# Kernel optimization log

Measured on AMD Instinct MI355X. Metric: run time of the kernel, lower is better.

The kernel has to match this reference:

```python
import jax, jax.numpy as jnp
import numpy as np

NF = 16            # num_frequencies
S = 2              # scale_factor
MAX_STD = 0.5
POS_LIMIT = 1.0


def setup_inputs() -> dict:
    key = jax.random.key(0)
    ks = jax.random.split(key, 8)
    B, G, H, W = 16, 256, 128, 128
    hidden, base = 1024, 256
    in_dim = (G + 2 * NF + 1) * S * S  # 4624
    # xavier-uniform-like scales
    lim1 = float(np.sqrt(6.0 / (hidden + in_dim)))
    lim2 = float(np.sqrt(6.0 / (base + hidden)))
    return {
        "position": jax.random.uniform(ks[0], (B, 4), dtype=jnp.float32),
        "gestalt": jax.random.normal(ks[1], (B, G), dtype=jnp.float32),
        "mask": jax.random.uniform(ks[2], (B, 1, H, W), dtype=jnp.float32),
        "depth": jax.random.normal(ks[3], (B, 1, H, W), dtype=jnp.float32),
        "weight1": jax.random.uniform(ks[4], (hidden, in_dim), minval=-lim1, maxval=lim1, dtype=jnp.float32),
        "bias1": jnp.zeros((hidden,), dtype=jnp.float32),
        "weight2": jax.random.uniform(ks[5], (base, hidden), minval=-lim2, maxval=lim2, dtype=jnp.float32),
        "bias2": jnp.zeros((base,), dtype=jnp.float32),
    }


def reference(position, gestalt, mask, depth, weight1, bias1, weight2, bias2):
    B, _, H, W = mask.shape
    # positional grids in [-1, 1], shapes (1,1,H,W)
    gx = (jnp.arange(W, dtype=jnp.float32) / (W - 1)) * 2 - 1
    gy = (jnp.arange(H, dtype=jnp.float32) / (H - 1)) * 2 - 1
    grid_y, grid_x = jnp.meshgrid(gy, gx, indexing="ij")
    grid_x = grid_x[None, None]
    grid_y = grid_y[None, None]

    x = jnp.clip(position[:, 0], -POS_LIMIT, POS_LIMIT)[:, None, None, None]
    y = jnp.clip(position[:, 1], -POS_LIMIT, POS_LIMIT)[:, None, None, None]
    min_std = 1.0 / min(H, W)
    std = 0.1 / jnp.clip(position[:, 3], min_std, MAX_STD)[:, None, None, None]
    std_y = std
    std_x = std * (W / H)

    half_pi = jnp.float32(np.pi / 2)
    ngx = (grid_x - x) * std_x * half_pi  # (B,1,H,W)
    ngy = (grid_y - y) * std_y * half_pi
    freqs = (2.0 ** jnp.arange(NF, dtype=jnp.float32))[None, :, None, None]
    cos_x = jnp.cos(ngx * freqs)  # (B,NF,H,W)
    cos_y = jnp.cos(ngy * freqs)
    # interleave: [cx0, cy0, cx1, cy1, ...]
    embedding = jnp.stack([cos_x, cos_y], axis=2).reshape(B, 2 * NF, H, W)

    inp = jnp.concatenate(
        [gestalt[:, :, None, None] * mask, embedding * mask, depth * mask], axis=1
    )  # (B,C,H,W)
    C = inp.shape[1]
    # space-to-depth patchify
    p = inp.reshape(B, C, H // S, S, W // S, S)
    p = p.transpose(0, 2, 4, 1, 3, 5).reshape(B * (H // S) * (W // S), C * S * S)

    h = p @ weight1.T + bias1
    h = h * jax.nn.sigmoid(h)  # SiLU
    o = h @ weight2.T + bias2
    return o.reshape(B, H // S, W // S, -1).transpose(0, 3, 1, 2)
```

## Files before the change

kernel.cpp:

```cpp
#include <hip/hip_runtime.h>
#include <cstdio>


#define NFREQ 16
#define BB 16
#define G 256
#define KIN 1156
#define K1 144
#define STAGE_U16 12800
#define NSTAGE 3

typedef unsigned short u16;
using bf16x8 = __bf16 __attribute__((ext_vector_type(8)));
using f32x16 = float __attribute__((ext_vector_type(16)));
using f32x4  = float __attribute__((ext_vector_type(4)));

__device__ __forceinline__ u16 f2bf(float f) {
  unsigned u = __float_as_uint(f);
  u += 0x7fffu + ((u >> 16) & 1u);
  return (u16)(u >> 16);
}
__device__ __forceinline__ unsigned pk2(float a, float b) {
  return (unsigned)f2bf(a) | ((unsigned)f2bf(b) << 16);
}
__device__ __forceinline__ unsigned pk2f(float a, float b) {
  unsigned ua = __float_as_uint(a) + 0x8000u;
  unsigned ub = __float_as_uint(b) + 0x8000u;
  return __builtin_amdgcn_perm(ub, ua, 0x07060302u);
}
__device__ __forceinline__ float silu(float h) {
  float e = __builtin_amdgcn_exp2f(h * -1.44269504088896f);
  return h * __builtin_amdgcn_rcpf(1.f + e);
}
__device__ __forceinline__ void gl_lds16(const u16* g, u16* l) {
  __builtin_amdgcn_global_load_lds(
      (const __attribute__((address_space(1))) void*)g,
      (__attribute__((address_space(3))) void*)l, 16, 0, 0);
}

__global__ void k_pre(const float* __restrict__ pos,
                      const float* __restrict__ gestalt,
                      const float* __restrict__ w1,
                      const float* __restrict__ w2,
                      const float* __restrict__ bias1,
                      float* __restrict__ cosx, float* __restrict__ cosy,
                      u16* __restrict__ B1F, u16* __restrict__ W2F) {
  const int bid = blockIdx.x;
  const int t = threadIdx.x;

  if (bid < 1024) {
    __shared__ float w1row[KIN];
    __shared__ float gestT[G * 17];
    __shared__ float psum[256];
    __shared__ float wg[64];
    const int n = bid;
    const float b1v = bias1[n];
#pragma unroll
    for (int i = t; i < KIN; i += 256) w1row[i] = w1[(size_t)n * KIN + i];
#pragma unroll
    for (int i = t; i < BB * G; i += 256) {
      int bb = i >> 8, c = i & 255;
      gestT[c * 17 + bb] = gestalt[i];
    }
    __syncthreads();
    {
      int bb = t & 15, j = (t >> 4) & 3, q = t >> 6;
      float acc = 0.f;
#pragma unroll 8
      for (int c = q * 64; c < q * 64 + 64; ++c)
        acc += gestT[c * 17 + bb] * w1row[4 * c + j];
      psum[t] = acc;
    }
    __syncthreads();
    if (t < 64) {
      int bb = t >> 2, j = t & 3;
      wg[t] = psum[j * 16 + bb] + psum[64 + j * 16 + bb] +
              psum[128 + j * 16 + bb] + psum[192 + j * 16 + bb];
    }
    __syncthreads();
    const int ch = n >> 5, l31n = n & 31;
    for (int c = t; c < BB * (K1 / 8); c += 256) {
      int bb = c / 18, kc = c - bb * 18;
      int k0 = kc * 8;
      float v[8];
#pragma unroll
      for (int i = 0; i < 8; ++i) {
        int k = k0 + i;
        float vv;
        if (k < 64)       vv = w1row[1024 + 8 * (k >> 2) + (k & 3)];
        else if (k < 128) { int kk = k - 64; vv = w1row[1024 + 8 * (kk >> 2) + 4 + (kk & 3)]; }
        else if (k < 132) vv = wg[bb * 4 + (k - 128)];
        else if (k < 136) vv = w1row[1152 + (k - 132)];
        else if (k == 136) vv = b1v;
        else              vv = 0.f;
        v[i] = vv;
      }
      uint4 u;
      u.x = pk2(v[0], v[1]); u.y = pk2(v[2], v[3]);
      u.z = pk2(v[4], v[5]); u.w = pk2(v[6], v[7]);
      size_t idx0 = ((((size_t)bb * 32 + ch) * 9 + (kc >> 1)) * 64 +
                     (kc & 1) * 32 + l31n) * 8;
      *(uint4*)(B1F + idx0) = u;
    }
  } else if (bid < 1152) {
    int e8 = (bid - 1024) * 256 + t;
    int lane = e8 & 63;
    int ct   = (e8 >> 6) & 7;
    int kc   = e8 >> 9;
    int n2 = ct * 32 + (lane & 31);
    int k2 = kc * 16 + (lane >> 5) * 8;
    const float* src = w2 + (size_t)n2 * 1024 + k2;
    uint4 u;
    u.x = pk2(src[0], src[1]); u.y = pk2(src[2], src[3]);
    u.z = pk2(src[4], src[5]); u.w = pk2(src[6], src[7]);
    *(uint4*)(W2F + (size_t)e8 * 8) = u;
  } else {
    int idx = (bid - 1152) * 256 + t;
    int table = idx >> 15;
    int rem = idx & 32767;
    int b = rem >> 11;
    int f = (rem >> 7) & 15;
    int c = rem & 127;
    float p0 = pos[b * 4 + 0];
    float p1 = pos[b * 4 + 1];
    float p3 = pos[b * 4 + 3];
    float x = fminf(fmaxf(p0, -1.f), 1.f);
    float y = fminf(fmaxf(p1, -1.f), 1.f);
    float stdv = 0.1f / fminf(fmaxf(p3, 0.0078125f), 0.5f);
    const float half_pi = 1.57079632679489661923f;
    float g = ((float)c / 127.0f) * 2.0f - 1.0f;
    float ng = (table == 0) ? ((g - x) * stdv) * half_pi
                            : ((g - y) * stdv) * half_pi;
    float freq = (float)(1 << f);
    float val = cosf(ng * freq);
    if (table == 0) cosx[(b * NFREQ + f) * 128 + c] = val;
    else            cosy[(b * NFREQ + f) * 128 + c] = val;
  }
}


__device__ __forceinline__ f32x16 mfma_bf16(bf16x8 a, bf16x8 b, f32x16 c) {
  return __builtin_amdgcn_mfma_f32_32x32x16_bf16(a, b, c, 0, 0, 0);
}

__device__ __forceinline__ void gemm1(const u16* afb, const bf16x8* bfr, int lane8,
                                      const f32x16& ZERO, f32x16& a1a, f32x16& a1b) {
  bf16x8 af0 = *(const bf16x8*)(afb + 0 * 512 + lane8);
  bf16x8 af1 = *(const bf16x8*)(afb + 1 * 512 + lane8);
  a1a = mfma_bf16(af0, bfr[0], ZERO);
  a1b = mfma_bf16(af1, bfr[1], ZERO);
#pragma unroll
  for (int ks = 1; ks < 4; ++ks) {
    bf16x8 afa = *(const bf16x8*)(afb + (2 * ks) * 512 + lane8);
    bf16x8 afc = *(const bf16x8*)(afb + (2 * ks + 1) * 512 + lane8);
    a1a = mfma_bf16(afa, bfr[2 * ks], a1a);
    a1b = mfma_bf16(afc, bfr[2 * ks + 1], a1b);
  }
  bf16x8 af8 = *(const bf16x8*)(afb + 8 * 512 + lane8);
  a1a = mfma_bf16(af8, bfr[8], a1a);
}

__device__ __forceinline__ void gemm2(const u16* wfb, int lane8,
                                      bf16x8 fA, bf16x8 fB, f32x16* acc2) {
#pragma unroll
  for (int ct = 0; ct < 8; ++ct) {
    bf16x8 wf = *(const bf16x8*)(wfb + ct * 512 + lane8);
    acc2[ct] = mfma_bf16(fA, wf, acc2[ct]);
  }
#pragma unroll
  for (int ct = 0; ct < 8; ++ct) {
    bf16x8 wf = *(const bf16x8*)(wfb + 4096 + ct * 512 + lane8);
    acc2[ct] = mfma_bf16(fB, wf, acc2[ct]);
  }
}

__device__ __forceinline__ void silupack(const f32x16& a1a, const f32x16& a1b,
                                         bf16x8& fragA, bf16x8& fragB) {
  unsigned d[8];
#pragma unroll
  for (int q = 0; q < 4; ++q) {
    float s0 = silu(a1a[4 * q + 0] + a1b[4 * q + 0]);
    float s1 = silu(a1a[4 * q + 1] + a1b[4 * q + 1]);
    float s2 = silu(a1a[4 * q + 2] + a1b[4 * q + 2]);
    float s3 = silu(a1a[4 * q + 3] + a1b[4 * q + 3]);
    d[2 * q]     = pk2f(s0, s1);
    d[2 * q + 1] = pk2f(s2, s3);
  }
  unsigned e0 = d[0], e1 = d[2];
  unsigned e2 = d[1], e3 = d[3];
  unsigned e4 = d[4], e5 = d[6];
  unsigned e6 = d[5], e7 = d[7];
  asm("v_permlane32_swap_b32 %0, %1" : "+v"(e0), "+v"(e1));
  asm("v_permlane32_swap_b32 %0, %1" : "+v"(e2), "+v"(e3));
  asm("v_permlane32_swap_b32 %0, %1" : "+v"(e4), "+v"(e5));
  asm("v_permlane32_swap_b32 %0, %1" : "+v"(e6), "+v"(e7));
  uint4 fav, fbv;
  fav.x = e0; fav.y = e2; fav.z = e1; fav.w = e3;
  fbv.x = e4; fbv.y = e6; fbv.z = e5; fbv.w = e7;
  fragA = __builtin_bit_cast(bf16x8, fav);
  fragB = __builtin_bit_cast(bf16x8, fbv);
}

__global__ __launch_bounds__(256, 2) void k_main(
    const u16* __restrict__ B1F, const u16* __restrict__ W2F,
    const float* __restrict__ mask, const float* __restrict__ depth,
    const float* __restrict__ cosx, const float* __restrict__ cosy,
    const float* __restrict__ bias2, float* __restrict__ out)
{
  __shared__ __align__(16) u16 sbuf[NSTAGE * STAGE_U16];
  float* stg = (float*)sbuf;

  const int tid = threadIdx.x;
  const int w = tid >> 6;
  const int lane = tid & 63;
  const int lane8 = lane * 8;
  const int l31 = lane & 31;
  const int lhi = lane >> 5;
  const int bswz = (blockIdx.x & 7) * 64 + (blockIdx.x >> 3);
  const int r0 = bswz * 128;
  const int b = r0 >> 12;
  const int oy0 = (r0 >> 6) & 63;

  {
    const float4* cx4 = (const float4*)(cosx + (size_t)b * 2048);
    ((float4*)stg)[tid]       = cx4[tid];
    ((float4*)stg)[tid + 256] = cx4[tid + 256];
    if (tid < 64)
      stg[2048 + tid] = cosy[((size_t)b * 16 + (tid >> 2)) * 128 + 2 * oy0 + (tid & 3)];
    if (tid < 128) {
      ((float4*)(stg + 2112))[tid] = ((const float4*)(mask  + ((size_t)b * 128 + 2 * oy0) * 128))[tid];
      ((float4*)(stg + 2624))[tid] = ((const float4*)(depth + ((size_t)b * 128 + 2 * oy0) * 128))[tid];
    }
  }
  __syncthreads();

  bf16x8 bfr[9];
  {
    const int r = w * 32 + l31;
    const int oyl = r >> 6, ox = r & 63;
    float m[4], dd[4];
#pragma unroll
    for (int j = 0; j < 4; ++j) {
      int sy = j >> 1, sx = j & 1;
      float mv = stg[2112 + (2 * oyl + sy) * 128 + 2 * ox + sx];
      m[j] = mv;
      dd[j] = stg[2624 + (2 * oyl + sy) * 128 + 2 * ox + sx] * mv;
    }
#pragma unroll
    for (int ks = 0; ks < 9; ++ks) {
      const int k0 = ks * 16 + lhi * 8;
      unsigned dwords[4];
#pragma unroll
      for (int h = 0; h < 4; ++h) {
        float v[2];
#pragma unroll
        for (int p = 0; p < 2; ++p) {
          const int k = k0 + 2 * h + p;
          float vv;
          if (k < 64) {
            const int f = k >> 2, j = k & 3;
            vv = m[j] * stg[f * 128 + 2 * ox + (j & 1)];
          } else if (k < 128) {
            const int kk = k - 64, f = kk >> 2, j = kk & 3;
            vv = m[j] * stg[2048 + f * 4 + 2 * oyl + (j >> 1)];
          } else if (k < 132) {
            vv = m[k - 128];
          } else if (k < 136) {
            vv = dd[k - 132];
          } else if (k == 136) {
            vv = 1.0f;
          } else {
            vv = 0.f;
          }
          v[p] = vv;
        }
        dwords[h] = pk2(v[0], v[1]);
      }
      uint4 u; u.x = dwords[0]; u.y = dwords[1]; u.z = dwords[2]; u.w = dwords[3];
      bfr[ks] = __builtin_bit_cast(bf16x8, u);
    }
  }
  __syncthreads();

  f32x16 acc2[8];
#pragma unroll
  for (int c = 0; c < 8; ++c)
#pragma unroll
    for (int i = 0; i < 16; ++i) acc2[c][i] = 0.f;

  f32x16 ZERO;
#pragma unroll
  for (int i = 0; i < 16; ++i) ZERO[i] = 0.f;

  const int naf = (w == 0) ? 3 : 2;
  const int wf0 = 9 + ((w + 3) & 3);
  const u16* apre = B1F + (size_t)b * 32 * 4608 + lane8;
  const u16* wpre = W2F + lane8;

  auto prefetchP = [&](u16* dst) {
#pragma unroll
    for (int j = 0; j < 3; ++j)
      if (j < naf) gl_lds16(apre + (w + 4 * j) * 512, dst + (w + 4 * j) * 512);
#pragma unroll
    for (int j = 0; j < 4; ++j) {
      const int c = wf0 + 4 * j;
      gl_lds16(wpre + (c - 9) * 512, dst + c * 512);
    }
    apre += 4608; wpre += 8192;
  };

  prefetchP(sbuf);
  prefetchP(sbuf + STAGE_U16);
  asm volatile("s_waitcnt vmcnt(6)" ::: "memory");
  __builtin_amdgcn_s_barrier();
  asm volatile("" ::: "memory");
  __builtin_amdgcn_sched_barrier(0);

  bf16x8 fragA, fragB;

  {
    f32x16 a1a, a1b;
    __builtin_amdgcn_s_setprio(1);
    gemm1(sbuf, bfr, lane8, ZERO, a1a, a1b);
    __builtin_amdgcn_s_setprio(0);
    asm volatile("s_waitcnt vmcnt(0)" ::: "memory");
    __builtin_amdgcn_s_barrier();
    asm volatile("" ::: "memory");
    __builtin_amdgcn_sched_barrier(0);
    prefetchP(sbuf + 2 * STAGE_U16);
    silupack(a1a, a1b, fragA, fragB);
  }

  int st = 1;
  for (int ch = 1; ch < 32; ++ch) {
    const u16* afb  = sbuf + st * STAGE_U16;
    const int  stp  = (st == 0) ? 2 : st - 1;
    const u16* wfbp = sbuf + stp * STAGE_U16 + 4608;

    f32x16 a1a, a1b;
    __builtin_amdgcn_s_setprio(1);
    gemm1(afb, bfr, lane8, ZERO, a1a, a1b);
    gemm2(wfbp, lane8, fragA, fragB, acc2);
    __builtin_amdgcn_s_setprio(0);

    asm volatile("s_waitcnt vmcnt(0)" ::: "memory");
    __builtin_amdgcn_s_barrier();
    asm volatile("" ::: "memory");
    __builtin_amdgcn_sched_barrier(0);

    if (ch + 2 < 32) {
      int s2 = st + 2; if (s2 >= NSTAGE) s2 -= NSTAGE;
      prefetchP(sbuf + s2 * STAGE_U16);
    }

    silupack(a1a, a1b, fragA, fragB);
    if (++st == NSTAGE) st = 0;
  }

  gemm2(sbuf + 1 * STAGE_U16 + 4608, lane8, fragA, fragB, acc2);

#pragma unroll
  for (int ct = 0; ct < 8; ++ct) {
    const int n2 = ct * 32 + l31;
    const float b2 = bias2[n2];
    float* ob = out + ((size_t)b * 256 + n2) * 4096;
#pragma unroll
    for (int q = 0; q < 4; ++q) {
      const int rl = w * 32 + 8 * q + 4 * lhi;
      const int oy = oy0 + (rl >> 6);
      const int ox = rl & 63;
      f32x4 v;
      v[0] = acc2[ct][4 * q + 0] + b2;
      v[1] = acc2[ct][4 * q + 1] + b2;
      v[2] = acc2[ct][4 * q + 2] + b2;
      v[3] = acc2[ct][4 * q + 3] + b2;
      *(f32x4*)(ob + oy * 64 + ox) = v;
    }
  }
}


extern "C" void kernel_launch(void* const* d_in, const int* in_sizes, int n_in,
                              void* d_out, int out_size, void* d_ws, size_t ws_size,
                              hipStream_t stream) {
  const float* pos     = (const float*)d_in[0];
  const float* gestalt = (const float*)d_in[1];
  const float* mask    = (const float*)d_in[2];
  const float* depth   = (const float*)d_in[3];
  const float* w1      = (const float*)d_in[4];
  const float* bias1   = (const float*)d_in[5];
  const float* w2      = (const float*)d_in[6];
  const float* bias2   = (const float*)d_in[7];
  float* out = (float*)d_out;

  const size_t NEED = 131072u + 131072u + 4718592u + 524288u;
  if (ws_size < NEED) {
    fprintf(stderr, "[kernel] ws_size=%zu < needed %zu — skipping launches\n",
            ws_size, NEED);
    return;
  }
  char* ws = (char*)d_ws;
  float* cosx = (float*)(ws);
  float* cosy = (float*)(ws + 131072);
  u16*   B1F  = (u16*)(ws + 262144);
  u16*   W2F  = (u16*)(ws + 262144 + 4718592);

  k_pre<<<1408, 256, 0, stream>>>(pos, gestalt, w1, w2, bias1, cosx, cosy, B1F, W2F);
  k_main<<<512, 256, 0, stream>>>(B1F, W2F, mask, depth, cosx, cosy, bias2, out);
}
```

Measured before the change: 158.4 us.

## Use 512-thread blocks with a six-stage pipeline and barriers every two chunks

Doubles the work per block from 128 to 256 output rows using eight waves, halving the grid to 256 blocks. This halves how often each W1/W2 weight chunk is reloaded across blocks. The LDS ring grows from three to six stages so prefetch runs three chunks ahead, and the full vmcnt(0)+barrier per chunk becomes a partial wait with a barrier every other chunk. The roughly 150 KB of LDS limits each CU to one block, so latency hiding relies on the deeper prefetch and the eight waves within one block rather than on a second co-resident block.

```diff
diff --git a/kernel.cpp b/kernel.cpp
--- a/kernel.cpp
+++ b/kernel.cpp
@@ -8,7 +8,7 @@
 #define KIN 1156
 #define K1 144
 #define STAGE_U16 12800
-#define NSTAGE 3
+#define NSTAGE 6
 
 typedef unsigned short u16;
 using bf16x8 = __bf16 __attribute__((ext_vector_type(8)));
@@ -201,7 +201,7 @@
   fragB = __builtin_bit_cast(bf16x8, fbv);
 }
 
-__global__ __launch_bounds__(256, 2) void k_main(
+__global__ __launch_bounds__(512, 2) void k_main(
     const u16* __restrict__ B1F, const u16* __restrict__ W2F,
     const float* __restrict__ mask, const float* __restrict__ depth,
     const float* __restrict__ cosx, const float* __restrict__ cosy,
@@ -216,20 +216,19 @@
   const int lane8 = lane * 8;
   const int l31 = lane & 31;
   const int lhi = lane >> 5;
-  const int bswz = (blockIdx.x & 7) * 64 + (blockIdx.x >> 3);
-  const int r0 = bswz * 128;
+  const int bswz = (blockIdx.x & 7) * 32 + (blockIdx.x >> 3);
+  const int r0 = bswz * 256;
   const int b = r0 >> 12;
   const int oy0 = (r0 >> 6) & 63;
 
   {
     const float4* cx4 = (const float4*)(cosx + (size_t)b * 2048);
-    ((float4*)stg)[tid]       = cx4[tid];
-    ((float4*)stg)[tid + 256] = cx4[tid + 256];
-    if (tid < 64)
-      stg[2048 + tid] = cosy[((size_t)b * 16 + (tid >> 2)) * 128 + 2 * oy0 + (tid & 3)];
-    if (tid < 128) {
-      ((float4*)(stg + 2112))[tid] = ((const float4*)(mask  + ((size_t)b * 128 + 2 * oy0) * 128))[tid];
-      ((float4*)(stg + 2624))[tid] = ((const float4*)(depth + ((size_t)b * 128 + 2 * oy0) * 128))[tid];
+    ((float4*)stg)[tid] = cx4[tid];
+    if (tid < 128)
+      stg[2048 + tid] = cosy[((size_t)b * 16 + (tid >> 3)) * 128 + 2 * oy0 + (tid & 7)];
+    if (tid < 256) {
+      ((float4*)(stg + 2176))[tid] = ((const float4*)(mask  + ((size_t)b * 128 + 2 * oy0) * 128))[tid];
+      ((float4*)(stg + 3200))[tid] = ((const float4*)(depth + ((size_t)b * 128 + 2 * oy0) * 128))[tid];
     }
   }
   __syncthreads();
@@ -242,9 +241,9 @@
 #pragma unroll
     for (int j = 0; j < 4; ++j) {
       int sy = j >> 1, sx = j & 1;
-      float mv = stg[2112 + (2 * oyl + sy) * 128 + 2 * ox + sx];
+      float mv = stg[2176 + (2 * oyl + sy) * 128 + 2 * ox + sx];
       m[j] = mv;
-      dd[j] = stg[2624 + (2 * oyl + sy) * 128 + 2 * ox + sx] * mv;
+      dd[j] = stg[3200 + (2 * oyl + sy) * 128 + 2 * ox + sx] * mv;
     }
 #pragma unroll
     for (int ks = 0; ks < 9; ++ks) {
@@ -262,7 +261,7 @@
             vv = m[j] * stg[f * 128 + 2 * ox + (j & 1)];
           } else if (k < 128) {
             const int kk = k - 64, f = kk >> 2, j = kk & 3;
-            vv = m[j] * stg[2048 + f * 4 + 2 * oyl + (j >> 1)];
+            vv = m[j] * stg[2048 + f * 8 + 2 * oyl + (j >> 1)];
           } else if (k < 132) {
             vv = m[k - 128];
           } else if (k < 136) {
@@ -292,49 +291,54 @@
 #pragma unroll
   for (int i = 0; i < 16; ++i) ZERO[i] = 0.f;
 
-  const int naf = (w == 0) ? 3 : 2;
-  const int wf0 = 9 + ((w + 3) & 3);
   const u16* apre = B1F + (size_t)b * 32 * 4608 + lane8;
   const u16* wpre = W2F + lane8;
 
   auto prefetchP = [&](u16* dst) {
-#pragma unroll
-    for (int j = 0; j < 3; ++j)
-      if (j < naf) gl_lds16(apre + (w + 4 * j) * 512, dst + (w + 4 * j) * 512);
-#pragma unroll
-    for (int j = 0; j < 4; ++j) {
-      const int c = wf0 + 4 * j;
-      gl_lds16(wpre + (c - 9) * 512, dst + c * 512);
-    }
+    gl_lds16(apre + w * 512, dst + w * 512);
+    if (w == 7) gl_lds16(apre + 8 * 512, dst + 8 * 512);
+    gl_lds16(wpre + w * 512, dst + (9 + w) * 512);
+    gl_lds16(wpre + (8 + w) * 512, dst + (17 + w) * 512);
     apre += 4608; wpre += 8192;
   };
 
   prefetchP(sbuf);
   prefetchP(sbuf + STAGE_U16);
-  asm volatile("s_waitcnt vmcnt(6)" ::: "memory");
-  __builtin_amdgcn_s_barrier();
-  asm volatile("" ::: "memory");
-  __builtin_amdgcn_sched_barrier(0);
+  prefetchP(sbuf + 2 * STAGE_U16);
 
   bf16x8 fragA, fragB;
 
   {
+    if (w == 7) asm volatile("s_waitcnt vmcnt(4)" ::: "memory");
+    else        asm volatile("s_waitcnt vmcnt(3)" ::: "memory");
+    __builtin_amdgcn_s_barrier();
+    asm volatile("" ::: "memory");
+    __builtin_amdgcn_sched_barrier(0);
+    prefetchP(sbuf + 3 * STAGE_U16);
+
     f32x16 a1a, a1b;
     __builtin_amdgcn_s_setprio(1);
     gemm1(sbuf, bfr, lane8, ZERO, a1a, a1b);
     __builtin_amdgcn_s_setprio(0);
-    asm volatile("s_waitcnt vmcnt(0)" ::: "memory");
-    __builtin_amdgcn_s_barrier();
-    asm volatile("" ::: "memory");
-    __builtin_amdgcn_sched_barrier(0);
-    prefetchP(sbuf + 2 * STAGE_U16);
     silupack(a1a, a1b, fragA, fragB);
   }
 
   int st = 1;
+  int stw = 4;
   for (int ch = 1; ch < 32; ++ch) {
+    if (!(ch & 1)) {
+      if (ch == 30) asm volatile("s_waitcnt vmcnt(0)" ::: "memory");
+      else if (w == 7) asm volatile("s_waitcnt vmcnt(4)" ::: "memory");
+      else             asm volatile("s_waitcnt vmcnt(3)" ::: "memory");
+      __builtin_amdgcn_s_barrier();
+      asm volatile("" ::: "memory");
+      __builtin_amdgcn_sched_barrier(0);
+    }
+    if (ch + 3 < 32) prefetchP(sbuf + stw * STAGE_U16);
+    stw = (stw + 1 == NSTAGE) ? 0 : stw + 1;
+
     const u16* afb  = sbuf + st * STAGE_U16;
-    const int  stp  = (st == 0) ? 2 : st - 1;
+    const int  stp  = (st == 0) ? NSTAGE - 1 : st - 1;
     const u16* wfbp = sbuf + stp * STAGE_U16 + 4608;
 
     f32x16 a1a, a1b;
@@ -343,18 +347,8 @@
     gemm2(wfbp, lane8, fragA, fragB, acc2);
     __builtin_amdgcn_s_setprio(0);
 
-    asm volatile("s_waitcnt vmcnt(0)" ::: "memory");
-    __builtin_amdgcn_s_barrier();
-    asm volatile("" ::: "memory");
-    __builtin_amdgcn_sched_barrier(0);
-
-    if (ch + 2 < 32) {
-      int s2 = st + 2; if (s2 >= NSTAGE) s2 -= NSTAGE;
-      prefetchP(sbuf + s2 * STAGE_U16);
-    }
-
     silupack(a1a, a1b, fragA, fragB);
-    if (++st == NSTAGE) st = 0;
+    st = (st + 1 == NSTAGE) ? 0 : st + 1;
   }
 
   gemm2(sbuf + 1 * STAGE_U16 + 4608, lane8, fragA, fragB, acc2);
@@ -406,5 +400,5 @@
   u16*   W2F  = (u16*)(ws + 262144 + 4718592);
 
   k_pre<<<1408, 256, 0, stream>>>(pos, gestalt, w1, w2, bias1, cosx, cosy, B1F, W2F);
-  k_main<<<512, 256, 0, stream>>>(B1F, W2F, mask, depth, cosx, cosy, bias2, out);
-}
+  k_main<<<256, 512, 0, stream>>>(B1F, W2F, mask, depth, cosx, cosy, bias2, out);
+}
```

Result: no change. 156.5 us (-1.2%).

## Warp-specialize k_main into GEMM1 producer and GEMM2 consumer wave groups

Applied to the files above, without the earlier changes.

The block grows from 4 to 12 waves. Four waves compute GEMM1 plus SiLU and hand packed bf16 fragments through a double-buffered LDS region. Eight waves consume them for GEMM2, each pair splitting the output columns in half. The LDS pipeline goes from 3 to 4 stages, and each group issues its own global-to-LDS loads. This is meant to overlap GEMM1 and GEMM2 across waves instead of serializing them in one wave, at the cost of extra LDS traffic for the fragments, more LDS per block, and fragile hand-counted vmcnt/barrier matching between the two groups.

```diff
diff --git a/kernel.cpp b/kernel.cpp
--- a/kernel.cpp
+++ b/kernel.cpp
@@ -8,7 +8,8 @@
 #define KIN 1156
 #define K1 144
 #define STAGE_U16 12800
-#define NSTAGE 3
+#define NSTAGE 4
+#define SB_U16 (NSTAGE * STAGE_U16)
 
 typedef unsigned short u16;
 using bf16x8 = __bf16 __attribute__((ext_vector_type(8)));
@@ -160,22 +161,8 @@
   a1a = mfma_bf16(af8, bfr[8], a1a);
 }
 
-__device__ __forceinline__ void gemm2(const u16* wfb, int lane8,
-                                      bf16x8 fA, bf16x8 fB, f32x16* acc2) {
-#pragma unroll
-  for (int ct = 0; ct < 8; ++ct) {
-    bf16x8 wf = *(const bf16x8*)(wfb + ct * 512 + lane8);
-    acc2[ct] = mfma_bf16(fA, wf, acc2[ct]);
-  }
-#pragma unroll
-  for (int ct = 0; ct < 8; ++ct) {
-    bf16x8 wf = *(const bf16x8*)(wfb + 4096 + ct * 512 + lane8);
-    acc2[ct] = mfma_bf16(fB, wf, acc2[ct]);
-  }
-}
-
 __device__ __forceinline__ void silupack(const f32x16& a1a, const f32x16& a1b,
-                                         bf16x8& fragA, bf16x8& fragB) {
+                                         uint4& fav, uint4& fbv) {
   unsigned d[8];
 #pragma unroll
   for (int q = 0; q < 4; ++q) {
@@ -194,37 +181,32 @@
   asm("v_permlane32_swap_b32 %0, %1" : "+v"(e2), "+v"(e3));
   asm("v_permlane32_swap_b32 %0, %1" : "+v"(e4), "+v"(e5));
   asm("v_permlane32_swap_b32 %0, %1" : "+v"(e6), "+v"(e7));
-  uint4 fav, fbv;
   fav.x = e0; fav.y = e2; fav.z = e1; fav.w = e3;
   fbv.x = e4; fbv.y = e6; fbv.z = e5; fbv.w = e7;
-  fragA = __builtin_bit_cast(bf16x8, fav);
-  fragB = __builtin_bit_cast(bf16x8, fbv);
-}
-
-__global__ __launch_bounds__(256, 2) void k_main(
+}
+
+__global__ __launch_bounds__(768, 3) void k_main(
     const u16* __restrict__ B1F, const u16* __restrict__ W2F,
     const float* __restrict__ mask, const float* __restrict__ depth,
     const float* __restrict__ cosx, const float* __restrict__ cosy,
     const float* __restrict__ bias2, float* __restrict__ out)
 {
-  __shared__ __align__(16) u16 sbuf[NSTAGE * STAGE_U16];
+  __shared__ __align__(16) u16 sbuf[NSTAGE * STAGE_U16 + 8192];
   float* stg = (float*)sbuf;
 
   const int tid = threadIdx.x;
-  const int w = tid >> 6;
+  const int wid = tid >> 6;
   const int lane = tid & 63;
   const int lane8 = lane * 8;
   const int l31 = lane & 31;
   const int lhi = lane >> 5;
   const int bswz = (blockIdx.x & 7) * 64 + (blockIdx.x >> 3);
-  const int r0 = bswz * 128;
-  const int b = r0 >> 12;
-  const int oy0 = (r0 >> 6) & 63;
+  const int b = bswz >> 5;
+  const int oy0 = (bswz * 2) & 63;
 
   {
     const float4* cx4 = (const float4*)(cosx + (size_t)b * 2048);
-    ((float4*)stg)[tid]       = cx4[tid];
-    ((float4*)stg)[tid + 256] = cx4[tid + 256];
+    if (tid < 512) ((float4*)stg)[tid] = cx4[tid];
     if (tid < 64)
       stg[2048 + tid] = cosy[((size_t)b * 16 + (tid >> 2)) * 128 + 2 * oy0 + (tid & 3)];
     if (tid < 128) {
@@ -234,146 +216,175 @@
   }
   __syncthreads();
 
-  bf16x8 bfr[9];
-  {
-    const int r = w * 32 + l31;
-    const int oyl = r >> 6, ox = r & 63;
-    float m[4], dd[4];
-#pragma unroll
-    for (int j = 0; j < 4; ++j) {
-      int sy = j >> 1, sx = j & 1;
-      float mv = stg[2112 + (2 * oyl + sy) * 128 + 2 * ox + sx];
-      m[j] = mv;
-      dd[j] = stg[2624 + (2 * oyl + sy) * 128 + 2 * ox + sx] * mv;
-    }
-#pragma unroll
-    for (int ks = 0; ks < 9; ++ks) {
-      const int k0 = ks * 16 + lhi * 8;
-      unsigned dwords[4];
-#pragma unroll
-      for (int h = 0; h < 4; ++h) {
-        float v[2];
-#pragma unroll
-        for (int p = 0; p < 2; ++p) {
-          const int k = k0 + 2 * h + p;
-          float vv;
-          if (k < 64) {
-            const int f = k >> 2, j = k & 3;
-            vv = m[j] * stg[f * 128 + 2 * ox + (j & 1)];
-          } else if (k < 128) {
-            const int kk = k - 64, f = kk >> 2, j = kk & 3;
-            vv = m[j] * stg[2048 + f * 4 + 2 * oyl + (j >> 1)];
-          } else if (k < 132) {
-            vv = m[k - 128];
-          } else if (k < 136) {
-            vv = dd[k - 132];
-          } else if (k == 136) {
-            vv = 1.0f;
-          } else {
-            vv = 0.f;
+  u16* const SB = sbuf + SB_U16;
+
+  if (wid >= 8) {
+    const int hh = wid - 8;
+    bf16x8 bfr[9];
+    {
+      const int r = hh * 32 + l31;
+      const int oyl = r >> 6, ox = r & 63;
+      float m[4], dd[4];
+#pragma unroll
+      for (int j = 0; j < 4; ++j) {
+        int sy = j >> 1, sx = j & 1;
+        float mv = stg[2112 + (2 * oyl + sy) * 128 + 2 * ox + sx];
+        m[j] = mv;
+        dd[j] = stg[2624 + (2 * oyl + sy) * 128 + 2 * ox + sx] * mv;
+      }
+#pragma unroll
+      for (int ks = 0; ks < 9; ++ks) {
+        const int k0 = ks * 16 + lhi * 8;
+        unsigned dwords[4];
+#pragma unroll
+        for (int h = 0; h < 4; ++h) {
+          float v[2];
+#pragma unroll
+          for (int p = 0; p < 2; ++p) {
+            const int k = k0 + 2 * h + p;
+            float vv;
+            if (k < 64) {
+              const int f = k >> 2, j = k & 3;
+              vv = m[j] * stg[f * 128 + 2 * ox + (j & 1)];
+            } else if (k < 128) {
+              const int kk = k - 64, f = kk >> 2, j = kk & 3;
+              vv = m[j] * stg[2048 + f * 4 + 2 * oyl + (j >> 1)];
+            } else if (k < 132) {
+              vv = m[k - 128];
+            } else if (k < 136) {
+              vv = dd[k - 132];
+            } else if (k == 136) {
+              vv = 1.0f;
+            } else {
+              vv = 0.f;
+            }
+            v[p] = vv;
           }
-          v[p] = vv;
+          dwords[h] = pk2(v[0], v[1]);
         }
-        dwords[h] = pk2(v[0], v[1]);
+        uint4 u; u.x = dwords[0]; u.y = dwords[1]; u.z = dwords[2]; u.w = dwords[3];
+        bfr[ks] = __builtin_bit_cast(bf16x8, u);
       }
-      uint4 u; u.x = dwords[0]; u.y = dwords[1]; u.z = dwords[2]; u.w = dwords[3];
-      bfr[ks] = __builtin_bit_cast(bf16x8, u);
-    }
-  }
+    }
+    __syncthreads();
+
+    f32x16 ZERO;
+#pragma unroll
+    for (int i = 0; i < 16; ++i) ZERO[i] = 0.f;
+
+    const u16* apre = B1F + (size_t)b * 147456 + lane8;
+    auto issueH = [&](u16* dst) {
+      gl_lds16(apre + hh * 512, dst + hh * 512);
+      gl_lds16(apre + (4 + hh) * 512, dst + (4 + hh) * 512);
+      if (hh == 0) gl_lds16(apre + 8 * 512, dst + 8 * 512);
+      apre += 4608;
+    };
+    issueH(sbuf);
+    issueH(sbuf + STAGE_U16);
+    issueH(sbuf + 2 * STAGE_U16);
+
+    __syncthreads();
+
+    {
+      f32x16 a1a, a1b;
+      gemm1(sbuf, bfr, lane8, ZERO, a1a, a1b);
+      uint4 fav, fbv;
+      silupack(a1a, a1b, fav, fbv);
+      u16* sd = SB + hh * 1024 + lane8;
+      *(uint4*)(sd) = fav;
+      *(uint4*)(sd + 512) = fbv;
+    }
+    __syncthreads();
+
+    for (int ch = 0; ch < 32; ++ch) {
+      if (ch <= 29) {
+        if (hh == 0) asm volatile("s_waitcnt vmcnt(3)" ::: "memory");
+        else         asm volatile("s_waitcnt vmcnt(2)" ::: "memory");
+      } else {
+        asm volatile("s_waitcnt vmcnt(0)" ::: "memory");
+      }
+      __builtin_amdgcn_s_barrier();
+      asm volatile("" ::: "memory");
+      __builtin_amdgcn_sched_barrier(0);
+
+      if (ch <= 28) issueH(sbuf + ((ch + 3) & 3) * STAGE_U16);
+
+      if (ch + 1 < 32) {
+        const u16* afb = sbuf + ((ch + 1) & 3) * STAGE_U16;
+        f32x16 a1a, a1b;
+        gemm1(afb, bfr, lane8, ZERO, a1a, a1b);
+        uint4 fav, fbv;
+        silupack(a1a, a1b, fav, fbv);
+        u16* sd = SB + ((ch + 1) & 1) * 4096 + hh * 1024 + lane8;
+        *(uint4*)(sd) = fav;
+        *(uint4*)(sd + 512) = fbv;
+      }
+      asm volatile("s_waitcnt lgkmcnt(0)" ::: "memory");
+    }
+    return;
+  }
+
+  const int pair = wid >> 1, half = wid & 1;
   __syncthreads();
 
-  f32x16 acc2[8];
-#pragma unroll
-  for (int c = 0; c < 8; ++c)
+  f32x16 acc2[4];
+#pragma unroll
+  for (int c = 0; c < 4; ++c)
 #pragma unroll
     for (int i = 0; i < 16; ++i) acc2[c][i] = 0.f;
 
-  f32x16 ZERO;
-#pragma unroll
-  for (int i = 0; i < 16; ++i) ZERO[i] = 0.f;
-
-  const int naf = (w == 0) ? 3 : 2;
-  const int wf0 = 9 + ((w + 3) & 3);
-  const u16* apre = B1F + (size_t)b * 32 * 4608 + lane8;
   const u16* wpre = W2F + lane8;
-
-  auto prefetchP = [&](u16* dst) {
-#pragma unroll
-    for (int j = 0; j < 3; ++j)
-      if (j < naf) gl_lds16(apre + (w + 4 * j) * 512, dst + (w + 4 * j) * 512);
-#pragma unroll
-    for (int j = 0; j < 4; ++j) {
-      const int c = wf0 + 4 * j;
-      gl_lds16(wpre + (c - 9) * 512, dst + c * 512);
-    }
-    apre += 4608; wpre += 8192;
+  auto issueC = [&](u16* dst) {
+    gl_lds16(wpre + wid * 512, dst + 4608 + wid * 512);
+    gl_lds16(wpre + (8 + wid) * 512, dst + 4608 + (8 + wid) * 512);
+    wpre += 8192;
   };
-
-  prefetchP(sbuf);
-  prefetchP(sbuf + STAGE_U16);
-  asm volatile("s_waitcnt vmcnt(6)" ::: "memory");
-  __builtin_amdgcn_s_barrier();
-  asm volatile("" ::: "memory");
-  __builtin_amdgcn_sched_barrier(0);
-
-  bf16x8 fragA, fragB;
-
-  {
-    f32x16 a1a, a1b;
-    __builtin_amdgcn_s_setprio(1);
-    gemm1(sbuf, bfr, lane8, ZERO, a1a, a1b);
-    __builtin_amdgcn_s_setprio(0);
-    asm volatile("s_waitcnt vmcnt(0)" ::: "memory");
+  issueC(sbuf);
+  issueC(sbuf + STAGE_U16);
+  issueC(sbuf + 2 * STAGE_U16);
+
+  __syncthreads();
+  __syncthreads();
+
+  for (int ch = 0; ch < 32; ++ch) {
+    if (ch <= 29)      asm volatile("s_waitcnt vmcnt(4)" ::: "memory");
+    else if (ch == 30) asm volatile("s_waitcnt vmcnt(2)" ::: "memory");
+    else               asm volatile("s_waitcnt vmcnt(0)" ::: "memory");
     __builtin_amdgcn_s_barrier();
     asm volatile("" ::: "memory");
     __builtin_amdgcn_sched_barrier(0);
-    prefetchP(sbuf + 2 * STAGE_U16);
-    silupack(a1a, a1b, fragA, fragB);
-  }
-
-  int st = 1;
-  for (int ch = 1; ch < 32; ++ch) {
-    const u16* afb  = sbuf + st * STAGE_U16;
-    const int  stp  = (st == 0) ? 2 : st - 1;
-    const u16* wfbp = sbuf + stp * STAGE_U16 + 4608;
-
-    f32x16 a1a, a1b;
-    __builtin_amdgcn_s_setprio(1);
-    gemm1(afb, bfr, lane8, ZERO, a1a, a1b);
-    gemm2(wfbp, lane8, fragA, fragB, acc2);
-    __builtin_amdgcn_s_setprio(0);
-
-    asm volatile("s_waitcnt vmcnt(0)" ::: "memory");
-    __builtin_amdgcn_s_barrier();
-    asm volatile("" ::: "memory");
-    __builtin_amdgcn_sched_barrier(0);
-
-    if (ch + 2 < 32) {
-      int s2 = st + 2; if (s2 >= NSTAGE) s2 -= NSTAGE;
-      prefetchP(sbuf + s2 * STAGE_U16);
-    }
-
-    silupack(a1a, a1b, fragA, fragB);
-    if (++st == NSTAGE) st = 0;
-  }
-
-  gemm2(sbuf + 1 * STAGE_U16 + 4608, lane8, fragA, fragB, acc2);
-
-#pragma unroll
-  for (int ct = 0; ct < 8; ++ct) {
-    const int n2 = ct * 32 + l31;
+
+    if (ch <= 28) issueC(sbuf + ((ch + 3) & 3) * STAGE_U16);
+
+    const u16* sS = SB + (ch & 1) * 4096 + pair * 1024 + lane8;
+    bf16x8 fragA = *(const bf16x8*)(sS);
+    bf16x8 fragB = *(const bf16x8*)(sS + 512);
+    const u16* wfb = sbuf + (ch & 3) * STAGE_U16 + 4608;
+#pragma unroll
+    for (int q = 0; q < 4; ++q) {
+      const int ct = half * 4 + q;
+      bf16x8 wlo = *(const bf16x8*)(wfb + ct * 512 + lane8);
+      acc2[q] = mfma_bf16(fragA, wlo, acc2[q]);
+      bf16x8 whi = *(const bf16x8*)(wfb + 4096 + ct * 512 + lane8);
+      acc2[q] = mfma_bf16(fragB, whi, acc2[q]);
+    }
+  }
+
+#pragma unroll
+  for (int qn = 0; qn < 4; ++qn) {
+    const int n2 = half * 128 + qn * 32 + l31;
     const float b2 = bias2[n2];
     float* ob = out + ((size_t)b * 256 + n2) * 4096;
 #pragma unroll
     for (int q = 0; q < 4; ++q) {
-      const int rl = w * 32 + 8 * q + 4 * lhi;
+      const int rl = pair * 32 + 8 * q + 4 * lhi;
       const int oy = oy0 + (rl >> 6);
       const int ox = rl & 63;
       f32x4 v;
-      v[0] = acc2[ct][4 * q + 0] + b2;
-      v[1] = acc2[ct][4 * q + 1] + b2;
-      v[2] = acc2[ct][4 * q + 2] + b2;
-      v[3] = acc2[ct][4 * q + 3] + b2;
+      v[0] = acc2[qn][4 * q + 0] + b2;
+      v[1] = acc2[qn][4 * q + 1] + b2;
+      v[2] = acc2[qn][4 * q + 2] + b2;
+      v[3] = acc2[qn][4 * q + 3] + b2;
       *(f32x4*)(ob + oy * 64 + ox) = v;
     }
   }
@@ -406,5 +417,5 @@
   u16*   W2F  = (u16*)(ws + 262144 + 4718592);
 
   k_pre<<<1408, 256, 0, stream>>>(pos, gestalt, w1, w2, bias1, cosx, cosy, B1F, W2F);
-  k_main<<<512, 256, 0, stream>>>(B1F, W2F, mask, depth, cosx, cosy, bias2, out);
-}
+  k_main<<<512, 768, 0, stream>>>(B1F, W2F, mask, depth, cosx, cosy, bias2, out);
+}
```

New measurement: 171.5 us. 8.2% more time.
